# Kernel tuning notes

Measured on AMD Instinct MI355X. Metric: run time of the kernel, lower is better.

## Reference

```python
import jax, jax.numpy as jnp
import numpy as np

B, T, H, NH = 16, 2048, 1024, 16
HD = H // NH  # 64
IN0, IN1 = 256, 512  # modality input sizes needing projection; modality 2 is already H


def _ln(x, g, b, eps=1e-5):
    m = jnp.mean(x, axis=-1, keepdims=True)
    v = jnp.mean((x - m) ** 2, axis=-1, keepdims=True)
    return (x - m) / jnp.sqrt(v + eps) * g + b


def setup_inputs() -> dict:
    key = jax.random.key(0)
    ks = jax.random.split(key, 24)
    s = 0.02
    d = {
        'x0': jax.random.normal(ks[0], (B, T, IN0), jnp.float32),
        'x1': jax.random.normal(ks[1], (B, T, IN1), jnp.float32),
        'x2': jax.random.normal(ks[2], (B, T, H), jnp.float32),
        'static_context': jax.random.normal(ks[3], (B, T, H), jnp.float32),
        'Wp0': jax.random.normal(ks[4], (H, IN0), jnp.float32) * s,
        'bp0': jnp.zeros((H,), jnp.float32),
        'Wp1': jax.random.normal(ks[5], (H, IN1), jnp.float32) * s,
        'bp1': jnp.zeros((H,), jnp.float32),
        'Wq': jax.random.normal(ks[6], (H, H), jnp.float32) * s,
        'bq': jnp.zeros((H,), jnp.float32),
        'Wk': jax.random.normal(ks[7], (H, H), jnp.float32) * s,
        'bk': jnp.zeros((H,), jnp.float32),
        'Wv': jax.random.normal(ks[8], (H, H), jnp.float32) * s,
        'bv': jnp.zeros((H,), jnp.float32),
        'Wo': jax.random.normal(ks[9], (H, H), jnp.float32) * s,
        'bo': jnp.zeros((H,), jnp.float32),
        'query_token': jax.random.normal(ks[10], (H,), jnp.float32) * s,
        'g1': jnp.ones((H,), jnp.float32),
        'be1': jnp.zeros((H,), jnp.float32),
        'g2': jnp.ones((H,), jnp.float32),
        'be2': jnp.zeros((H,), jnp.float32),
        'W1': jax.random.normal(ks[11], (4 * H, H), jnp.float32) * s,
        'b1': jnp.zeros((4 * H,), jnp.float32),
        'W2': jax.random.normal(ks[12], (H, 4 * H), jnp.float32) * s,
        'b2': jnp.zeros((H,), jnp.float32),
    }
    return d


def _forward(x0, x1, x2, static_context, Wp0, bp0, Wp1, bp1, Wq, bq, Wk, bk, Wv, bv,
             Wo, bo, query_token, g1, be1, g2, be2, W1, b1, W2, b2):
    # project modalities to hidden size, stack -> [B, T, M, H]
    m0 = x0 @ Wp0.T + bp0
    m1 = x1 @ Wp1.T + bp1
    stacked = jnp.stack([m0, m1, x2], axis=2)  # [B,T,3,H]
    M = stacked.shape[2]
    # per-timestep single-query cross-attention over the M modality tokens,
    # batched over all B*T positions (equivalent to the torch per-t loop)
    q = query_token + static_context  # [B,T,H]
    Q = (q @ Wq.T + bq).reshape(B, T, NH, HD)
    K = (stacked @ Wk.T + bk).reshape(B, T, M, NH, HD)
    V = (stacked @ Wv.T + bv).reshape(B, T, M, NH, HD)
    scores = jnp.einsum('bthd,btmhd->bthm', Q, K) / jnp.sqrt(jnp.asarray(HD, Q.dtype))
    attn = jax.nn.softmax(scores, axis=-1)  # [B,T,NH,M]
    weights = attn.mean(axis=2)  # average over heads (torch default) -> [B,T,M]
    ctx = jnp.einsum('bthm,btmhd->bthd', attn, V).reshape(B, T, H)
    attn_out = ctx @ Wo.T + bo
    fused = _ln(attn_out, g1, be1)
    ff = jax.nn.gelu(fused @ W1.T + b1, approximate=False) @ W2.T + b2
    fused = _ln(fused + ff, g2, be2)
    return fused, weights


def reference(x0, x1, x2, static_context, Wp0, bp0, Wp1, bp1, Wq, bq, Wk, bk, Wv, bv,
              Wo, bo, query_token, g1, be1, g2, be2, W1, b1, W2, b2):
    return _forward(x0, x1, x2, static_context, Wp0, bp0, Wp1, bp1, Wq, bq, Wk, bk,
                    Wv, bv, Wo, bo, query_token, g1, be1, g2, be2, W1, b1, W2, b2)
```

## Files before the change

### kernel.cpp

```cpp
#include <hip/hip_runtime.h>
#include <hip/hip_bf16.h>
#include <math.h>

#define BT 32768
#define HH 1024

typedef unsigned short u16;
typedef __attribute__((ext_vector_type(4))) unsigned short u16x4;
typedef __attribute__((ext_vector_type(8))) unsigned short u16x8;
typedef __attribute__((ext_vector_type(8))) __bf16 bf16x8;
typedef __attribute__((ext_vector_type(4))) float f32x4;

#define DEVI static __device__ __forceinline__

DEVI u16 f2bf(float f){
  unsigned u = __builtin_bit_cast(unsigned, f);
  u += 0x7FFFu + ((u >> 16) & 1u);
  return (u16)(u >> 16);
}
DEVI float bf2f(u16 h){
  unsigned u = ((unsigned)h) << 16;
  return __builtin_bit_cast(float, u);
}
DEVI void gl_lds16(const void* g, void* l){
  __builtin_amdgcn_global_load_lds((const __attribute__((address_space(1))) void*)g,
                                   (__attribute__((address_space(3))) void*)l, 16, 0, 0);
}
DEVI int swz(int row, int elem){ return elem ^ ((row & 7) << 3); }

__global__ void k_cast4(const float* __restrict__ s, u16* __restrict__ d, int n4){
  int i = blockIdx.x*blockDim.x + threadIdx.x;
  int st = gridDim.x*blockDim.x;
  for (; i < n4; i += st){
    float4 v = ((const float4*)s)[i];
    u16x4 o = { f2bf(v.x), f2bf(v.y), f2bf(v.z), f2bf(v.w) };
    ((u16x4*)d)[i] = o;
  }
}

__global__ void k_qb(const float* __restrict__ qt, const float* __restrict__ sc,
                     u16* __restrict__ d, int n4){
  int i = blockIdx.x*blockDim.x + threadIdx.x;
  int st = gridDim.x*blockDim.x;
  for (; i < n4; i += st){
    int e = i*4; int c = e & 1023;
    float4 v = *(const float4*)&sc[e];
    float4 q = *(const float4*)&qt[c];
    u16x4 o = { f2bf(v.x+q.x), f2bf(v.y+q.y), f2bf(v.z+q.z), f2bf(v.w+q.w) };
    ((u16x4*)d)[i] = o;
  }
}

__global__ void k_copyf(const float* __restrict__ s, float* __restrict__ d, int n){
  int i = blockIdx.x*blockDim.x + threadIdx.x;
  int st = gridDim.x*blockDim.x;
  for (; i < n; i += st) d[i] = s[i];
}

__global__ void k_psm(const float* __restrict__ s, float* __restrict__ p,
                      float* __restrict__ wout, int T){
  int t = blockIdx.x*blockDim.x + threadIdx.x;
  int st = gridDim.x*blockDim.x;
  for (; t < T; t += st){
    float a0 = 0.f, a1 = 0.f, a2 = 0.f;
    #pragma unroll
    for (int h = 0; h < 16; ++h){
      const float* b = s + (size_t)t*48 + h*3;
      float s0 = b[0], s1 = b[1], s2 = b[2];
      float mx = fmaxf(s0, fmaxf(s1, s2));
      float e0 = __expf(s0-mx), e1 = __expf(s1-mx), e2 = __expf(s2-mx);
      float inv = 1.f/(e0+e1+e2);
      e0 *= inv; e1 *= inv; e2 *= inv;
      float* q = p + (size_t)t*48 + h*3;
      q[0] = e0; q[1] = e1; q[2] = e2;
      a0 += e0; a1 += e1; a2 += e2;
    }
    wout[(size_t)t*3+0] = a0*0.0625f;
    wout[(size_t)t*3+1] = a1*0.0625f;
    wout[(size_t)t*3+2] = a2*0.0625f;
  }
}

__global__ void k_transcast(const float* __restrict__ s, u16* __restrict__ d, int R, int C){
  __shared__ float tile[32][33];
  int c0 = blockIdx.x*32, r0 = blockIdx.y*32;
  int tx = threadIdx.x & 31, ty = threadIdx.x >> 5;
  #pragma unroll
  for (int i = 0; i < 32; i += 8) tile[ty+i][tx] = s[(size_t)(r0+ty+i)*C + c0+tx];
  __syncthreads();
  #pragma unroll
  for (int i = 0; i < 32; i += 8) d[(size_t)(c0+ty+i)*R + r0+tx] = f2bf(tile[tx][ty+i]);
}

__global__ void k_matvec(const u16* __restrict__ W, const float* __restrict__ x,
                         const float* __restrict__ badd, float* __restrict__ out, int K){
  int row = blockIdx.x*4 + (threadIdx.x>>6);
  int lane = threadIdx.x & 63;
  float s = 0.f;
  for (int k = lane; k < K; k += 64) s += bf2f(W[(size_t)row*K + k]) * x[k];
  #pragma unroll
  for (int m = 1; m < 64; m <<= 1) s += __shfl_xor(s, m);
  if (lane == 0) out[row] = s + badd[row];
}

__global__ __launch_bounds__(256, 3)
void k_gemm(const u16* __restrict__ A, int lda,
            const u16* __restrict__ B, int ldb, int K,
            const float* __restrict__ bias,
            u16* __restrict__ C, int ldc, int col0, int act)
{
  __shared__ u16 As[128*64];
  __shared__ u16 Bs[128*64];
  const int tid = threadIdx.x, lane = tid & 63, wid = tid >> 6;
  const int wr = wid >> 1, wc = wid & 1;
  const int r15 = lane & 15, g = lane >> 4;
  const int m0 = blockIdx.x * 128, n0 = blockIdx.y * 128;
  f32x4 acc[4][4] = {};

  for (int k0 = 0; k0 < K; k0 += 64){
    #pragma unroll
    for (int it = 0; it < 4; ++it){
      int c = it*256 + tid;
      int row = c >> 3;
      int ke = swz(row, (c & 7) * 8);
      gl_lds16(A + (size_t)(m0+row)*lda + (k0+ke), As + c*8);
      gl_lds16(B + (size_t)(n0+row)*ldb + (k0+ke), Bs + c*8);
    }
    __syncthreads();
    #pragma unroll
    for (int kk = 0; kk < 64; kk += 32){
      bf16x8 av[4], bvv[4];
      #pragma unroll
      for (int i = 0; i < 4; ++i){
        int row = wr*64 + i*16 + r15;
        av[i] = *(const bf16x8*)&As[row*64 + swz(row, kk + g*8)];
      }
      #pragma unroll
      for (int j = 0; j < 4; ++j){
        int row = wc*64 + j*16 + r15;
        bvv[j] = *(const bf16x8*)&Bs[row*64 + swz(row, kk + g*8)];
      }
      #pragma unroll
      for (int i = 0; i < 4; ++i)
        #pragma unroll
        for (int j = 0; j < 4; ++j)
          acc[i][j] = __builtin_amdgcn_mfma_f32_16x16x32_bf16(av[i], bvv[j], acc[i][j], 0, 0, 0);
    }
    __syncthreads();
  }
  #pragma unroll
  for (int j = 0; j < 4; ++j){
    int col = wc*64 + j*16 + r15;
    float bb = bias ? bias[n0 + col] : 0.f;
    #pragma unroll
    for (int i = 0; i < 4; ++i){
      #pragma unroll
      for (int jj = 0; jj < 4; ++jj){
        int row = wr*64 + i*16 + g*4 + jj;
        float v = acc[i][j][jj] + bb;
        if (act == 1) v = 0.5f * v * (1.f + erff(v * 0.70710678118654752f));
        C[(size_t)(m0+row)*ldc + col0 + n0 + col] = f2bf(v);
      }
    }
  }
}

__global__ __launch_bounds__(256, 3)
void k_attnp1(const u16* __restrict__ x0b, const u16* __restrict__ x1b, const u16* __restrict__ x2b,
              const u16* __restrict__ Wc0, const u16* __restrict__ Wc1, const u16* __restrict__ Wc2,
              const float* __restrict__ bc0, const float* __restrict__ bc1, const float* __restrict__ bc2,
              const u16* __restrict__ Qg, float* __restrict__ sbuf)
{
  __shared__ u16 As[128*64];
  __shared__ u16 Bs[128*64];
  const int tid = threadIdx.x, lane = tid & 63, wid = tid >> 6;
  const int wr = wid >> 1, wc = wid & 1;
  const int r15 = lane & 15, g = lane >> 4;
  const int bid = blockIdx.x;
  const int xcd = bid & 7, bn = (bid >> 3) & 7, btb = (bid >> 6) * 8 + xcd;
  const int t0 = btb * 128, n0 = bn * 128;

  const u16* Xs[3] = { x0b, x1b, x2b };
  const u16* Ws[3] = { Wc0, Wc1, Wc2 };
  const float* Bc[3] = { bc0, bc1, bc2 };
  const int Ks[3] = { 256, 512, 1024 };

  f32x4 acc[4][4] = {};

  #pragma unroll
  for (int m = 0; m < 3; ++m){
    const int K = Ks[m];
    const u16* X = Xs[m];
    const u16* W = Ws[m];
    for (int k0 = 0; k0 < K; k0 += 64){
      #pragma unroll
      for (int it = 0; it < 4; ++it){
        int c = it*256 + tid;
        int row = c >> 3;
        int ke = swz(row, (c & 7) * 8);
        gl_lds16(X + (size_t)(t0+row)*K + (k0+ke), As + c*8);
        gl_lds16(W + (size_t)(n0+row)*K + (k0+ke), Bs + c*8);
      }
      __syncthreads();
      #pragma unroll
      for (int kk = 0; kk < 64; kk += 32){
        bf16x8 av[4], bvv[4];
        #pragma unroll
        for (int i = 0; i < 4; ++i){
          int row = wr*64 + i*16 + r15;
          av[i] = *(const bf16x8*)&As[row*64 + swz(row, kk + g*8)];
        }
        #pragma unroll
        for (int j = 0; j < 4; ++j){
          int row = wc*64 + j*16 + r15;
          bvv[j] = *(const bf16x8*)&Bs[row*64 + swz(row, kk + g*8)];
        }
        #pragma unroll
        for (int i = 0; i < 4; ++i)
          #pragma unroll
          for (int j = 0; j < 4; ++j)
            acc[i][j] = __builtin_amdgcn_mfma_f32_16x16x32_bf16(av[i], bvv[j], acc[i][j], 0, 0, 0);
      }
      __syncthreads();
    }
    float bkc[4];
    #pragma unroll
    for (int j = 0; j < 4; ++j) bkc[j] = Bc[m][n0 + wc*64 + j*16 + r15];
    #pragma unroll
    for (int i = 0; i < 4; ++i){
      #pragma unroll
      for (int jj = 0; jj < 4; ++jj){
        int row = wr*64 + i*16 + g*4 + jj;
        const u16* qrow = Qg + (size_t)(t0+row)*1024 + n0 + wc*64 + r15;
        float sv = 0.f;
        #pragma unroll
        for (int j = 0; j < 4; ++j)
          sv += (acc[i][j][jj] + bkc[j]) * bf2f(qrow[j*16]);
        sv += __shfl_xor(sv, 1); sv += __shfl_xor(sv, 2);
        sv += __shfl_xor(sv, 4); sv += __shfl_xor(sv, 8);
        if (r15 == 0) sbuf[((size_t)(t0+row)*16 + bn*2 + wc)*3 + m] = sv * 0.125f;
      }
    }
    #pragma unroll
    for (int i = 0; i < 4; ++i)
      #pragma unroll
      for (int j = 0; j < 4; ++j)
        acc[i][j] = f32x4{0.f, 0.f, 0.f, 0.f};
  }
}

__global__ __launch_bounds__(256, 2)
void k_attnp2(const u16* __restrict__ x0b, const u16* __restrict__ x1b, const u16* __restrict__ x2b,
              const u16* __restrict__ Wc0, const u16* __restrict__ Wc1, const u16* __restrict__ Wc2,
              const float* __restrict__ bc0, const float* __restrict__ bc1, const float* __restrict__ bc2,
              const float* __restrict__ pbuf, u16* __restrict__ ctx)
{
  __shared__ u16 As[128*64];
  __shared__ u16 Bs[128*64];
  __shared__ float pl[768];
  const int tid = threadIdx.x, lane = tid & 63, wid = tid >> 6;
  const int wr = wid >> 1, wc = wid & 1;
  const int r15 = lane & 15, g = lane >> 4;
  const int bid = blockIdx.x;
  const int xcd = bid & 7, bn = (bid >> 3) & 7, btb = (bid >> 6) * 8 + xcd;
  const int t0 = btb * 128, n0 = bn * 128;

  const u16* Xs[3] = { x0b, x1b, x2b };
  const u16* Ws[3] = { Wc0, Wc1, Wc2 };
  const float* Bc[3] = { bc0, bc1, bc2 };
  const int Ks[3] = { 256, 512, 1024 };

  for (int idx = tid; idx < 768; idx += 256){
    int r = idx / 6, rem = idx - r*6;
    int h = rem / 3, m = rem - h*3;
    pl[idx] = pbuf[((size_t)(t0+r)*16 + bn*2 + h)*3 + m];
  }
  __syncthreads();

  f32x4 cx[4][4] = {};

  #pragma unroll
  for (int m = 0; m < 3; ++m){
    const int K = Ks[m];
    const u16* X = Xs[m];
    const u16* W = Ws[m] + (size_t)1024*K;
    f32x4 acc[4][4] = {};
    for (int k0 = 0; k0 < K; k0 += 64){
      #pragma unroll
      for (int it = 0; it < 4; ++it){
        int c = it*256 + tid;
        int row = c >> 3;
        int ke = swz(row, (c & 7) * 8);
        gl_lds16(X + (size_t)(t0+row)*K + (k0+ke), As + c*8);
        gl_lds16(W + (size_t)(n0+row)*K + (k0+ke), Bs + c*8);
      }
      __syncthreads();
      #pragma unroll
      for (int kk = 0; kk < 64; kk += 32){
        bf16x8 av[4], bvv[4];
        #pragma unroll
        for (int i = 0; i < 4; ++i){
          int row = wr*64 + i*16 + r15;
          av[i] = *(const bf16x8*)&As[row*64 + swz(row, kk + g*8)];
        }
        #pragma unroll
        for (int j = 0; j < 4; ++j){
          int row = wc*64 + j*16 + r15;
          bvv[j] = *(const bf16x8*)&Bs[row*64 + swz(row, kk + g*8)];
        }
        #pragma unroll
        for (int i = 0; i < 4; ++i)
          #pragma unroll
          for (int j = 0; j < 4; ++j)
            acc[i][j] = __builtin_amdgcn_mfma_f32_16x16x32_bf16(av[i], bvv[j], acc[i][j], 0, 0, 0);
      }
      __syncthreads();
    }
    float bvc[4];
    #pragma unroll
    for (int j = 0; j < 4; ++j) bvc[j] = Bc[m][1024 + n0 + wc*64 + j*16 + r15];
    #pragma unroll
    for (int i = 0; i < 4; ++i){
      #pragma unroll
      for (int jj = 0; jj < 4; ++jj){
        int row = wr*64 + i*16 + g*4 + jj;
        float p = pl[row*6 + wc*3 + m];
        #pragma unroll
        for (int j = 0; j < 4; ++j)
          cx[i][j][jj] += p * (acc[i][j][jj] + bvc[j]);
      }
    }
  }
  #pragma unroll
  for (int i = 0; i < 4; ++i){
    #pragma unroll
    for (int jj = 0; jj < 4; ++jj){
      int row = wr*64 + i*16 + g*4 + jj;
      #pragma unroll
      for (int j = 0; j < 4; ++j)
        ctx[(size_t)(t0+row)*1024 + n0 + wc*64 + j*16 + r15] = f2bf(cx[i][j][jj]);
    }
  }
}

__global__ __launch_bounds__(256)
void k_ln(const u16* __restrict__ X, const u16* __restrict__ R,
          const float* __restrict__ gam, const float* __restrict__ bet,
          u16* __restrict__ outb, float* __restrict__ outf)
{
  __shared__ float rs[4], rq[4];
  const int t = blockIdx.x, tid = threadIdx.x;
  const size_t base = (size_t)t*1024 + tid*4;
  u16x4 xv = *(const u16x4*)&X[base];
  float v[4];
  #pragma unroll
  for (int i = 0; i < 4; ++i) v[i] = bf2f(xv[i]);
  if (R){
    u16x4 rv = *(const u16x4*)&R[base];
    #pragma unroll
    for (int i = 0; i < 4; ++i) v[i] += bf2f(rv[i]);
  }
  float s = v[0]+v[1]+v[2]+v[3];
  float q = v[0]*v[0]+v[1]*v[1]+v[2]*v[2]+v[3]*v[3];
  #pragma unroll
  for (int m = 1; m < 64; m <<= 1){ s += __shfl_xor(s, m); q += __shfl_xor(q, m); }
  if ((tid & 63) == 0){ rs[tid>>6] = s; rq[tid>>6] = q; }
  __syncthreads();
  s = rs[0]+rs[1]+rs[2]+rs[3];
  q = rq[0]+rq[1]+rq[2]+rq[3];
  float mean = s * (1.f/1024.f);
  float var  = q * (1.f/1024.f) - mean*mean;
  float rstd = rsqrtf(var + 1e-5f);
  int c0 = tid*4;
  if (outb){
    u16x4 o;
    #pragma unroll
    for (int i = 0; i < 4; ++i) o[i] = f2bf((v[i]-mean)*rstd*gam[c0+i] + bet[c0+i]);
    *(u16x4*)&outb[base] = o;
  } else {
    float4 o;
    o.x = (v[0]-mean)*rstd*gam[c0+0] + bet[c0+0];
    o.y = (v[1]-mean)*rstd*gam[c0+1] + bet[c0+1];
    o.z = (v[2]-mean)*rstd*gam[c0+2] + bet[c0+2];
    o.w = (v[3]-mean)*rstd*gam[c0+3] + bet[c0+3];
    *(float4*)&outf[base] = o;
  }
}

extern "C" void kernel_launch(void* const* d_in, const int* in_sizes, int n_in,
                              void* d_out, int out_size, void* d_ws, size_t ws_size,
                              hipStream_t stream)
{
  (void)in_sizes; (void)n_in; (void)out_size;
  const float* x0  = (const float*)d_in[0];
  const float* x1  = (const float*)d_in[1];
  const float* x2  = (const float*)d_in[2];
  const float* sc  = (const float*)d_in[3];
  const float* Wp0 = (const float*)d_in[4];  const float* bp0 = (const float*)d_in[5];
  const float* Wp1 = (const float*)d_in[6];  const float* bp1 = (const float*)d_in[7];
  const float* Wq  = (const float*)d_in[8];  const float* bq  = (const float*)d_in[9];
  const float* Wk  = (const float*)d_in[10]; const float* bk  = (const float*)d_in[11];
  const float* Wv  = (const float*)d_in[12]; const float* bv  = (const float*)d_in[13];
  const float* Wo  = (const float*)d_in[14]; const float* bo  = (const float*)d_in[15];
  const float* qt  = (const float*)d_in[16];
  const float* g1  = (const float*)d_in[17]; const float* be1 = (const float*)d_in[18];
  const float* g2  = (const float*)d_in[19]; const float* be2 = (const float*)d_in[20];
  const float* W1  = (const float*)d_in[21]; const float* b1  = (const float*)d_in[22];
  const float* W2  = (const float*)d_in[23]; const float* b2  = (const float*)d_in[24];

  char* ws = (char*)d_ws;
  size_t off = 0;
  auto alloc = [&](size_t b)->char*{ char* p = ws + off; off += (b + 255) & ~(size_t)255; return p; };

  u16* Wqb   = (u16*)alloc((size_t)1024*1024*2);
  u16* Wob   = (u16*)alloc((size_t)1024*1024*2);
  u16* W1b   = (u16*)alloc((size_t)4096*1024*2);
  u16* W2b   = (u16*)alloc((size_t)1024*4096*2);
  u16* Wkvb  = (u16*)alloc((size_t)2048*1024*2);
  u16* Wp0t  = (u16*)alloc((size_t)256*1024*2);
  u16* Wp1t  = (u16*)alloc((size_t)512*1024*2);
  u16* Wkv0c = (u16*)alloc((size_t)2048*256*2);
  u16* Wkv1c = (u16*)alloc((size_t)2048*512*2);
  float* bc0 = (float*)alloc((size_t)2048*4);
  float* bc1 = (float*)alloc((size_t)2048*4);
  float* bc2 = (float*)alloc((size_t)2048*4);
  char* regX  = alloc((size_t)BT*(256+512+1024)*2);
  char* regQ1 = alloc((size_t)BT*1024*2);
  char* regQ2 = alloc((size_t)BT*1024*2);
  float* sbuf = (float*)alloc((size_t)BT*48*4);
  float* pbuf = (float*)alloc((size_t)BT*48*4);
  if (off > ws_size) return;

  u16* x0b = (u16*)regX;
  u16* x1b = (u16*)(regX + (size_t)BT*256*2);
  u16* x2b = (u16*)(regX + (size_t)BT*768*2);
  u16* aob  = (u16*)regX;
  u16* ff2b = (u16*)regX;
  u16* qb   = (u16*)regQ1;
  u16* ctxb = (u16*)regQ1;
  u16* f1b  = (u16*)regQ1;
  u16* Qb   = (u16*)regQ2;
  u16* ff1c = (u16*)regQ2;

  dim3 B256(256);
  auto cast4 = [&](const float* s, u16* d, int n, int grid){
    k_cast4<<<dim3(grid), B256, 0, stream>>>(s, d, n >> 2);
  };
  cast4(Wq, Wqb, 1024*1024, 1024);
  cast4(Wk, Wkvb, 1024*1024, 1024);
  cast4(Wv, Wkvb + (size_t)1024*1024, 1024*1024, 1024);
  cast4(Wo, Wob, 1024*1024, 1024);
  cast4(W1, W1b, 4096*1024, 1024);
  cast4(W2, W2b, 4096*1024, 1024);
  cast4(x0, x0b, BT*256, 1024);
  cast4(x1, x1b, BT*512, 1024);
  cast4(x2, x2b, BT*1024, 2048);
  k_transcast<<<dim3(8, 32),  B256, 0, stream>>>(Wp0, Wp0t, 1024, 256);
  k_transcast<<<dim3(16, 32), B256, 0, stream>>>(Wp1, Wp1t, 1024, 512);
  k_copyf<<<dim3(4), B256, 0, stream>>>(bk, bc2, 1024);
  k_copyf<<<dim3(4), B256, 0, stream>>>(bv, bc2 + 1024, 1024);
  k_matvec<<<dim3(512), B256, 0, stream>>>(Wkvb, bp0, bc2, bc0, 1024);
  k_matvec<<<dim3(512), B256, 0, stream>>>(Wkvb, bp1, bc2, bc1, 1024);
  k_qb<<<dim3(2048), B256, 0, stream>>>(qt, sc, qb, BT*256);

  k_gemm<<<dim3(16, 2), B256, 0, stream>>>(Wkvb, 1024, Wp0t, 1024, 1024, nullptr, Wkv0c, 256, 0, 0);
  k_gemm<<<dim3(16, 4), B256, 0, stream>>>(Wkvb, 1024, Wp1t, 1024, 1024, nullptr, Wkv1c, 512, 0, 0);

  k_gemm<<<dim3(BT/128, 8), B256, 0, stream>>>(qb, 1024, Wqb, 1024, 1024, bq, Qb, 1024, 0, 0);
  k_attnp1<<<dim3(BT/128*8), B256, 0, stream>>>(x0b, x1b, x2b, Wkv0c, Wkv1c, Wkvb,
                                                bc0, bc1, bc2, Qb, sbuf);
  k_psm<<<dim3(128), B256, 0, stream>>>(sbuf, pbuf, (float*)d_out + (size_t)BT*1024, BT);
  k_attnp2<<<dim3(BT/128*8), B256, 0, stream>>>(x0b, x1b, x2b, Wkv0c, Wkv1c, Wkvb,
                                                bc0, bc1, bc2, pbuf, ctxb);
  k_gemm<<<dim3(BT/128, 8), B256, 0, stream>>>(ctxb, 1024, Wob, 1024, 1024, bo, aob, 1024, 0, 0);
  k_ln<<<dim3(BT), B256, 0, stream>>>(aob, nullptr, g1, be1, f1b, nullptr);

  for (int c = 0; c < 4; ++c){
    const u16* fa = f1b + (size_t)c*8192*1024;
    k_gemm<<<dim3(64, 32), B256, 0, stream>>>(fa, 1024, W1b, 1024, 1024, b1, ff1c, 4096, 0, 1);
    k_gemm<<<dim3(64, 8),  B256, 0, stream>>>(ff1c, 4096, W2b, 4096, 4096, b2,
                                              ff2b + (size_t)c*8192*1024, 1024, 0, 0);
  }
  float* outf = (float*)d_out;
  k_ln<<<dim3(BT), B256, 0, stream>>>(ff2b, f1b, g2, be2, nullptr, outf);
}
```

Baseline: 1.582 ms.

## Fuse attention score, softmax and context passes into one kernel

Result: faster. 1.549 ms (-2.1%).

```diff
diff --git a/kernel.cpp b/kernel.cpp
--- a/kernel.cpp
+++ b/kernel.cpp
@@ -57,27 +57,15 @@
   for (; i < n; i += st) d[i] = s[i];
 }
 
-__global__ void k_psm(const float* __restrict__ s, float* __restrict__ p,
-                      float* __restrict__ wout, int T){
-  int t = blockIdx.x*blockDim.x + threadIdx.x;
+__global__ void k_wmean(const float* __restrict__ p, float* __restrict__ out, int n){
+  int i = blockIdx.x*blockDim.x + threadIdx.x;
   int st = gridDim.x*blockDim.x;
-  for (; t < T; t += st){
-    float a0 = 0.f, a1 = 0.f, a2 = 0.f;
-    #pragma unroll
-    for (int h = 0; h < 16; ++h){
-      const float* b = s + (size_t)t*48 + h*3;
-      float s0 = b[0], s1 = b[1], s2 = b[2];
-      float mx = fmaxf(s0, fmaxf(s1, s2));
-      float e0 = __expf(s0-mx), e1 = __expf(s1-mx), e2 = __expf(s2-mx);
-      float inv = 1.f/(e0+e1+e2);
-      e0 *= inv; e1 *= inv; e2 *= inv;
-      float* q = p + (size_t)t*48 + h*3;
-      q[0] = e0; q[1] = e1; q[2] = e2;
-      a0 += e0; a1 += e1; a2 += e2;
-    }
-    wout[(size_t)t*3+0] = a0*0.0625f;
-    wout[(size_t)t*3+1] = a1*0.0625f;
-    wout[(size_t)t*3+2] = a2*0.0625f;
+  for (; i < n; i += st){
+    int t = i/3, m = i - t*3;
+    float s = 0.f;
+    #pragma unroll
+    for (int h = 0; h < 16; ++h) s += p[(size_t)t*48 + h*3 + m];
+    out[i] = s * 0.0625f;
   }
 }
 
@@ -165,14 +153,15 @@
   }
 }
 
-__global__ __launch_bounds__(256, 3)
-void k_attnp1(const u16* __restrict__ x0b, const u16* __restrict__ x1b, const u16* __restrict__ x2b,
-              const u16* __restrict__ Wc0, const u16* __restrict__ Wc1, const u16* __restrict__ Wc2,
-              const float* __restrict__ bc0, const float* __restrict__ bc1, const float* __restrict__ bc2,
-              const u16* __restrict__ Qg, float* __restrict__ sbuf)
+__global__ __launch_bounds__(256, 2)
+void k_attnf(const u16* __restrict__ x0b, const u16* __restrict__ x1b, const u16* __restrict__ x2b,
+             const u16* __restrict__ Wc0, const u16* __restrict__ Wc1, const u16* __restrict__ Wc2,
+             const float* __restrict__ bc0, const float* __restrict__ bc1, const float* __restrict__ bc2,
+             const u16* __restrict__ Qg, u16* __restrict__ ctx, float* __restrict__ pbuf)
 {
   __shared__ u16 As[128*64];
   __shared__ u16 Bs[128*64];
+  __shared__ float Sl[2*128*3];
   const int tid = threadIdx.x, lane = tid & 63, wid = tid >> 6;
   const int wr = wid >> 1, wc = wid & 1;
   const int r15 = lane & 15, g = lane >> 4;
@@ -185,13 +174,23 @@
   const float* Bc[3] = { bc0, bc1, bc2 };
   const int Ks[3] = { 256, 512, 1024 };
 
-  f32x4 acc[4][4] = {};
+  float qreg[4][4][4];
+  #pragma unroll
+  for (int i = 0; i < 4; ++i)
+    #pragma unroll
+    for (int jj = 0; jj < 4; ++jj){
+      int row = wr*64 + i*16 + g*4 + jj;
+      const u16* qr = Qg + (size_t)(t0+row)*1024 + n0 + wc*64 + r15;
+      #pragma unroll
+      for (int j = 0; j < 4; ++j) qreg[i][jj][j] = bf2f(qr[j*16]);
+    }
 
   #pragma unroll
   for (int m = 0; m < 3; ++m){
     const int K = Ks[m];
     const u16* X = Xs[m];
     const u16* W = Ws[m];
+    f32x4 acc[4][4] = {};
     for (int k0 = 0; k0 < K; k0 += 64){
       #pragma unroll
       for (int it = 0; it < 4; ++it){
@@ -231,54 +230,34 @@
       #pragma unroll
       for (int jj = 0; jj < 4; ++jj){
         int row = wr*64 + i*16 + g*4 + jj;
-        const u16* qrow = Qg + (size_t)(t0+row)*1024 + n0 + wc*64 + r15;
         float sv = 0.f;
         #pragma unroll
         for (int j = 0; j < 4; ++j)
-          sv += (acc[i][j][jj] + bkc[j]) * bf2f(qrow[j*16]);
+          sv += (acc[i][j][jj] + bkc[j]) * qreg[i][jj][j];
         sv += __shfl_xor(sv, 1); sv += __shfl_xor(sv, 2);
         sv += __shfl_xor(sv, 4); sv += __shfl_xor(sv, 8);
-        if (r15 == 0) sbuf[((size_t)(t0+row)*16 + bn*2 + wc)*3 + m] = sv * 0.125f;
-      }
-    }
-    #pragma unroll
-    for (int i = 0; i < 4; ++i)
-      #pragma unroll
-      for (int j = 0; j < 4; ++j)
-        acc[i][j] = f32x4{0.f, 0.f, 0.f, 0.f};
-  }
-}
-
-__global__ __launch_bounds__(256, 2)
-void k_attnp2(const u16* __restrict__ x0b, const u16* __restrict__ x1b, const u16* __restrict__ x2b,
-              const u16* __restrict__ Wc0, const u16* __restrict__ Wc1, const u16* __restrict__ Wc2,
-              const float* __restrict__ bc0, const float* __restrict__ bc1, const float* __restrict__ bc2,
-              const float* __restrict__ pbuf, u16* __restrict__ ctx)
-{
-  __shared__ u16 As[128*64];
-  __shared__ u16 Bs[128*64];
-  __shared__ float pl[768];
-  const int tid = threadIdx.x, lane = tid & 63, wid = tid >> 6;
-  const int wr = wid >> 1, wc = wid & 1;
-  const int r15 = lane & 15, g = lane >> 4;
-  const int bid = blockIdx.x;
-  const int xcd = bid & 7, bn = (bid >> 3) & 7, btb = (bid >> 6) * 8 + xcd;
-  const int t0 = btb * 128, n0 = bn * 128;
-
-  const u16* Xs[3] = { x0b, x1b, x2b };
-  const u16* Ws[3] = { Wc0, Wc1, Wc2 };
-  const float* Bc[3] = { bc0, bc1, bc2 };
-  const int Ks[3] = { 256, 512, 1024 };
-
-  for (int idx = tid; idx < 768; idx += 256){
-    int r = idx / 6, rem = idx - r*6;
-    int h = rem / 3, m = rem - h*3;
-    pl[idx] = pbuf[((size_t)(t0+r)*16 + bn*2 + h)*3 + m];
+        if (r15 == 0) Sl[(wc*128 + row)*3 + m] = sv * 0.125f;
+      }
+    }
   }
   __syncthreads();
 
+  {
+    int h2 = tid >> 7, tt = tid & 127;
+    int base = (h2*128 + tt)*3;
+    float s0 = Sl[base+0], s1 = Sl[base+1], s2 = Sl[base+2];
+    float mx = fmaxf(s0, fmaxf(s1, s2));
+    float e0 = __expf(s0-mx), e1 = __expf(s1-mx), e2 = __expf(s2-mx);
+    float inv = 1.f/(e0+e1+e2);
+    e0 *= inv; e1 *= inv; e2 *= inv;
+    __syncthreads();
+    Sl[base+0] = e0; Sl[base+1] = e1; Sl[base+2] = e2;
+    float* pp = pbuf + ((size_t)(t0+tt)*16 + (bn*2 + h2))*3;
+    pp[0] = e0; pp[1] = e1; pp[2] = e2;
+  }
+  __syncthreads();
+
   f32x4 cx[4][4] = {};
-
   #pragma unroll
   for (int m = 0; m < 3; ++m){
     const int K = Ks[m];
@@ -324,7 +303,7 @@
       #pragma unroll
       for (int jj = 0; jj < 4; ++jj){
         int row = wr*64 + i*16 + g*4 + jj;
-        float p = pl[row*6 + wc*3 + m];
+        float p = Sl[(wc*128 + row)*3 + m];
         #pragma unroll
         for (int j = 0; j < 4; ++j)
           cx[i][j][jj] += p * (acc[i][j][jj] + bvc[j]);
@@ -427,7 +406,6 @@
   char* regX  = alloc((size_t)BT*(256+512+1024)*2);
   char* regQ1 = alloc((size_t)BT*1024*2);
   char* regQ2 = alloc((size_t)BT*1024*2);
-  float* sbuf = (float*)alloc((size_t)BT*48*4);
   float* pbuf = (float*)alloc((size_t)BT*48*4);
   if (off > ws_size) return;
 
@@ -467,11 +445,10 @@
   k_gemm<<<dim3(16, 4), B256, 0, stream>>>(Wkvb, 1024, Wp1t, 1024, 1024, nullptr, Wkv1c, 512, 0, 0);
 
   k_gemm<<<dim3(BT/128, 8), B256, 0, stream>>>(qb, 1024, Wqb, 1024, 1024, bq, Qb, 1024, 0, 0);
-  k_attnp1<<<dim3(BT/128*8), B256, 0, stream>>>(x0b, x1b, x2b, Wkv0c, Wkv1c, Wkvb,
-                                                bc0, bc1, bc2, Qb, sbuf);
-  k_psm<<<dim3(128), B256, 0, stream>>>(sbuf, pbuf, (float*)d_out + (size_t)BT*1024, BT);
-  k_attnp2<<<dim3(BT/128*8), B256, 0, stream>>>(x0b, x1b, x2b, Wkv0c, Wkv1c, Wkvb,
-                                                bc0, bc1, bc2, pbuf, ctxb);
+  k_attnf<<<dim3(BT/128*8), B256, 0, stream>>>(x0b, x1b, x2b, Wkv0c, Wkv1c, Wkvb,
+                                               bc0, bc1, bc2, Qb, ctxb, pbuf);
+  float* outf = (float*)d_out;
+  k_wmean<<<dim3(384), B256, 0, stream>>>(pbuf, outf + (size_t)BT*1024, BT*3);
   k_gemm<<<dim3(BT/128, 8), B256, 0, stream>>>(ctxb, 1024, Wob, 1024, 1024, bo, aob, 1024, 0, 0);
   k_ln<<<dim3(BT), B256, 0, stream>>>(aob, nullptr, g1, be1, f1b, nullptr);
 
@@ -481,6 +458,5 @@
     k_gemm<<<dim3(64, 8),  B256, 0, stream>>>(ff1c, 4096, W2b, 4096, 4096, b2,
                                               ff2b + (size_t)c*8192*1024, 1024, 0, 0);
   }
-  float* outf = (float*)d_out;
   k_ln<<<dim3(BT), B256, 0, stream>>>(ff2b, f1b, g2, be2, nullptr, outf);
 }
```
